# Performance work log

Hardware: AMD Instinct MI355X
Metric: run time of the kernel (lower is better)

## Reference

```python
import jax, jax.numpy as jnp
import numpy as np

# ---- config (CSA layer, layer_idx=0 of pattern 'CSA,HCA') ----
B, T, C = 2, 2048, 2048
NH, NKV = 16, 8
HD = C // NH            # 128 head dim
ROPE_DIM = HD // 2      # partial RoPE dims (rope_head_dim=0 default)
RATIO = 4               # csa_compress_ratio
G = T // RATIO          # compressed groups (T divisible by ratio -> no pad)
IDX_NH = NH
IDX_HD = max(8, C // NH // 2)  # 64
TOPK = 64               # index_topk
Q_RANK = C // 2         # _default_rank
O_RPG = C // 2          # o_proj rank_per_group, o_groups=1


def rms_norm(x, eps=1e-6):
    return x * jax.lax.rsqrt(jnp.mean(jnp.square(x), axis=-1, keepdims=True) + eps)


def _rope(x, cos, sin):
    d = x.shape[-1] // 2
    x1, x2 = x[..., :d], x[..., d:]
    return jnp.concatenate([x1 * cos + x2 * sin, -x1 * sin + x2 * cos], axis=-1)


def partial_rope(x, cos, sin):
    # rotate only the last ROPE_DIM dims; cos/sin: [..., ROPE_DIM//2]
    xn, xr = x[..., :-ROPE_DIM], x[..., -ROPE_DIM:]
    return jnp.concatenate([xn, _rope(xr, cos, sin)], axis=-1)


def setup_inputs() -> dict:
    key = jax.random.key(0)
    ks = jax.random.split(key, 16)
    s = 0.02
    x = jax.random.normal(ks[0], (B, T, C), jnp.float32)
    pos = jnp.arange(T, dtype=jnp.float32)
    inv = 10000.0 ** (-jnp.arange(0, HD // 2, dtype=jnp.float32) / (HD // 2))
    ang = pos[:, None] * inv[None, :]  # [T, HD//2]
    p = lambda i, shp: jax.random.normal(ks[i], shp, jnp.float32) * s
    return dict(
        x=x, cos=jnp.cos(ang), sin=jnp.sin(ang),
        q_a_w=p(1, (C, Q_RANK)), q_b_w=p(2, (Q_RANK, NH * HD)),
        ck_w=p(3, (C, NKV * HD)), cv_w=p(4, (C, NKV * HD)), cg_w=p(5, (C, NKV * HD)),
        c_ape=p(6, (RATIO, NKV, HD)),
        iq_w=p(7, (C, IDX_NH * IDX_HD)), ik_w=p(8, (C, IDX_NH * IDX_HD)),
        ig_w=p(9, (C, IDX_NH * IDX_HD)), i_ape=p(10, (RATIO, IDX_NH, IDX_HD)),
        sink=jnp.zeros((NH,), jnp.float32),
        o_wa=p(11, (1, O_RPG, C)), o_pb=p(12, (O_RPG, C)),
    )


def reference(x, cos, sin, q_a_w, q_b_w, ck_w, cv_w, cg_w, c_ape,
              iq_w, ik_w, ig_w, i_ape, sink, o_wa, o_pb):
    NEG = jnp.finfo(jnp.float32).min
    half = ROPE_DIM // 2
    # --- low-rank queries + partial RoPE ---
    q = (x @ q_a_w @ q_b_w).reshape(B, T, NH, HD)
    q = partial_rope(q, cos[None, :, None, :half], sin[None, :, None, :half])
    # --- GatedCompressor: learned gated pooling over blocks of RATIO ---
    k = (x @ ck_w).reshape(B, G, RATIO, NKV, HD)
    v = (x @ cv_w).reshape(B, G, RATIO, NKV, HD)
    g = (x @ cg_w).reshape(B, G, RATIO, NKV, HD) + c_ape[None, None]
    w = jax.nn.softmax(g, axis=2)
    ck = (k * w).sum(2)  # [B,G,NKV,HD]
    cv = (v * w).sum(2)
    group_ends = jnp.arange(RATIO - 1, T, RATIO)  # [G]
    ckr = partial_rope(ck, cos[group_ends][None, :, None, :half],
                       sin[group_ends][None, :, None, :half])
    # --- LightningIndexer: compressed indexer keys + per-token top-k groups ---
    ik = (x @ ik_w).reshape(B, G, RATIO, IDX_NH, IDX_HD)
    ig = (x @ ig_w).reshape(B, G, RATIO, IDX_NH, IDX_HD) + i_ape[None, None]
    iw = jax.nn.softmax(ig, axis=2)
    ikeys = rms_norm((ik * iw).sum(2))  # [B,G,IH,IHD]
    iq = rms_norm((x @ iq_w).reshape(B, T, IDX_NH, IDX_HD))
    iscore = jnp.einsum('bthd,bghd->bhtg', iq, ikeys) * IDX_HD ** -0.5
    iscore = iscore.mean(axis=1)  # [B,T,G]
    causal = group_ends[None, None, :] <= jnp.arange(T)[None, :, None]
    iscore = jnp.where(causal, iscore, NEG)
    sel = jax.lax.top_k(iscore, TOPK)[1]  # [B,T,K]
    bidx = jnp.arange(B)[:, None, None]
    tidx = jnp.arange(T)[None, :, None]
    mask = jnp.zeros((B, T, G), bool).at[bidx, tidx, sel].set(True) & causal
    # --- compressed sparse attention with sink, GQA expand ---
    rep = NH // NKV
    kk = jnp.repeat(ckr, rep, axis=2)  # [B,G,NH,HD]
    vv = jnp.repeat(cv, rep, axis=2)
    scores = jnp.einsum('bthd,bghd->bhtg', q, kk) * HD ** -0.5
    scores = jnp.where(mask[:, None], scores, NEG)
    sinkb = jnp.broadcast_to(sink.reshape(1, NH, 1, 1), (B, NH, T, 1))
    probs = jax.nn.softmax(jnp.concatenate([scores, sinkb], axis=-1), axis=-1)[..., :-1]
    out = jnp.einsum('bhtg,bghd->bthd', probs, vv).reshape(B, T, C)
    # --- GroupedOutputProjection (o_groups=1) ---
    h = jnp.einsum('btgd,grd->btgr', out.reshape(B, T, 1, C), o_wa).reshape(B, T, -1)
    return rms_norm(h) @ o_pb
```

## Files before the change

kernel.cpp:

```cpp
#include <hip/hip_runtime.h>
#include <hip/hip_bf16.h>
#include <math.h>

constexpr int Bn  = 2;
constexpr int Tn  = 2048;
constexpr int NHn = 16;
constexpr int NKVn= 8;
constexpr int Gn  = 512;
constexpr int TKn = 64;

typedef __attribute__((ext_vector_type(8))) __bf16 bf16x8;
typedef __attribute__((ext_vector_type(4))) __bf16 bf16x4;
typedef __attribute__((ext_vector_type(2))) __bf16 bf16x2;
typedef __attribute__((ext_vector_type(4))) float f32x4;

__device__ __forceinline__ void gload_lds16(const void* g, void* l) {
  __builtin_amdgcn_global_load_lds(
      (const __attribute__((address_space(1))) unsigned int*)g,
      (__attribute__((address_space(3))) unsigned int*)l, 16, 0, 0);
}

__global__ __launch_bounds__(256) void gemm_pipe_kvqa(
    const __bf16* __restrict__ A, const __bf16* __restrict__ Bt,
    float* __restrict__ Cf, __bf16* __restrict__ Cq)
{
  constexpr int K = 2048;
  constexpr int NT = K / 64;
  __shared__ __bf16 lds[2][2][2][128][32];
  const int tid = threadIdx.x;
  const int wid = tid >> 6, lane = tid & 63;
  const int wm = wid >> 1, wn = wid & 1;
  const int row0 = blockIdx.y * 128, col0 = blockIdx.x * 128;

  f32x4 acc[4][4];
  const f32x4 zero = {0.f, 0.f, 0.f, 0.f};
  #pragma unroll
  for (int i = 0; i < 4; ++i)
    #pragma unroll
    for (int j = 0; j < 4; ++j) acc[i][j] = zero;

  auto stage = [&](int kt, int p, int buf) {
    long k0 = (long)kt * 64 + p * 32;
    #pragma unroll
    for (int l = 0; l < 2; ++l) {
      int u = l * 256 + tid;
      int r = u >> 2, c4 = u & 3;
      long csrc = (long)((c4 ^ ((r >> 1) & 3)) * 8);
      gload_lds16(A  + (long)(row0 + r) * K + k0 + csrc, &lds[buf][0][p][r][c4 * 8]);
      gload_lds16(Bt + (long)(col0 + r) * K + k0 + csrc, &lds[buf][1][p][r][c4 * 8]);
    }
  };

  stage(0, 0, 0);
  stage(0, 1, 0);

  for (int kt = 0; kt < NT; ++kt) {
    const int buf = kt & 1;
    #pragma unroll
    for (int ph = 0; ph < 2; ++ph) {
      if (kt + 1 < NT) {
        stage(kt + 1, ph, buf ^ 1);
        asm volatile("s_waitcnt vmcnt(8)" ::: "memory");
      } else {
        if (ph == 0) asm volatile("s_waitcnt vmcnt(4)" ::: "memory");
        else         asm volatile("s_waitcnt vmcnt(0)" ::: "memory");
      }
      asm volatile("s_barrier" ::: "memory");
      bf16x8 af[4], bfr[4];
      #pragma unroll
      for (int mf = 0; mf < 4; ++mf) {
        int r = wm * 64 + mf * 16 + (lane & 15);
        int c4 = (lane >> 4) ^ ((r >> 1) & 3);
        af[mf] = *(const bf16x8*)&lds[buf][0][ph][r][c4 * 8];
      }
      #pragma unroll
      for (int nf = 0; nf < 4; ++nf) {
        int r = wn * 64 + nf * 16 + (lane & 15);
        int c4 = (lane >> 4) ^ ((r >> 1) & 3);
        bfr[nf] = *(const bf16x8*)&lds[buf][1][ph][r][c4 * 8];
      }
      __builtin_amdgcn_s_setprio(1);
      #pragma unroll
      for (int mf = 0; mf < 4; ++mf)
        #pragma unroll
        for (int nf = 0; nf < 4; ++nf)
          acc[mf][nf] = __builtin_amdgcn_mfma_f32_16x16x32_bf16(af[mf], bfr[nf], acc[mf][nf], 0, 0, 0);
      __builtin_amdgcn_s_setprio(0);
      asm volatile("s_barrier" ::: "memory");
    }
  }

  const int crow = (lane >> 4) * 4, ccol = lane & 15;
  const bool isQ = (col0 >= 3072);
  #pragma unroll
  for (int mf = 0; mf < 4; ++mf)
    #pragma unroll
    for (int nf = 0; nf < 4; ++nf)
      #pragma unroll
      for (int j = 0; j < 4; ++j) {
        long r = row0 + wm * 64 + mf * 16 + crow + j;
        long c = col0 + wn * 64 + nf * 16 + ccol;
        float v = acc[mf][nf][j];
        if (isQ) Cq[r * 1024 + (c - 3072)] = (__bf16)v;
        else     Cf[r * 3072 + c] = v;
      }
}

template<int EPI>
__global__ __launch_bounds__(256) void gemm_pipe(
    const __bf16* __restrict__ A, const __bf16* __restrict__ Bt,
    void* __restrict__ Cp, int N, int K,
    const float* __restrict__ cosb, const float* __restrict__ sinb,
    const float* __restrict__ rs)
{
  const int NT = K >> 6;
  __shared__ __bf16 lds[2][2][2][128][32];
  const int tid = threadIdx.x;
  const int wid = tid >> 6, lane = tid & 63;
  const int wm = wid >> 1, wn = wid & 1;
  const int row0 = blockIdx.y * 128, col0 = blockIdx.x * 128;

  f32x4 acc[4][4];
  const f32x4 zero = {0.f, 0.f, 0.f, 0.f};
  #pragma unroll
  for (int i = 0; i < 4; ++i)
    #pragma unroll
    for (int j = 0; j < 4; ++j) acc[i][j] = zero;

  auto stage = [&](int kt, int p, int buf) {
    long k0 = (long)kt * 64 + p * 32;
    #pragma unroll
    for (int l = 0; l < 2; ++l) {
      int u = l * 256 + tid;
      int r = u >> 2, c4 = u & 3;
      long csrc = (long)((c4 ^ ((r >> 1) & 3)) * 8);
      gload_lds16(A  + (long)(row0 + r) * K + k0 + csrc, &lds[buf][0][p][r][c4 * 8]);
      gload_lds16(Bt + (long)(col0 + r) * K + k0 + csrc, &lds[buf][1][p][r][c4 * 8]);
    }
  };

  stage(0, 0, 0);
  stage(0, 1, 0);

  for (int kt = 0; kt < NT; ++kt) {
    const int buf = kt & 1;
    #pragma unroll
    for (int ph = 0; ph < 2; ++ph) {
      if (kt + 1 < NT) {
        stage(kt + 1, ph, buf ^ 1);
        asm volatile("s_waitcnt vmcnt(8)" ::: "memory");
      } else {
        if (ph == 0) asm volatile("s_waitcnt vmcnt(4)" ::: "memory");
        else         asm volatile("s_waitcnt vmcnt(0)" ::: "memory");
      }
      asm volatile("s_barrier" ::: "memory");
      bf16x8 af[4], bfr[4];
      #pragma unroll
      for (int mf = 0; mf < 4; ++mf) {
        int r = wm * 64 + mf * 16 + (lane & 15);
        int c4 = (lane >> 4) ^ ((r >> 1) & 3);
        af[mf] = *(const bf16x8*)&lds[buf][0][ph][r][c4 * 8];
      }
      #pragma unroll
      for (int nf = 0; nf < 4; ++nf) {
        int r = wn * 64 + nf * 16 + (lane & 15);
        int c4 = (lane >> 4) ^ ((r >> 1) & 3);
        bfr[nf] = *(const bf16x8*)&lds[buf][1][ph][r][c4 * 8];
      }
      __builtin_amdgcn_s_setprio(1);
      #pragma unroll
      for (int mf = 0; mf < 4; ++mf)
        #pragma unroll
        for (int nf = 0; nf < 4; ++nf)
          acc[mf][nf] = __builtin_amdgcn_mfma_f32_16x16x32_bf16(af[mf], bfr[nf], acc[mf][nf], 0, 0, 0);
      __builtin_amdgcn_s_setprio(0);
      asm volatile("s_barrier" ::: "memory");
    }
  }

  const int crow = (lane >> 4) * 4, ccol = lane & 15;
  if constexpr (EPI == 1) {
    __bf16* C = (__bf16*)Cp;
    if (wn == 1) {
      #pragma unroll
      for (int mf = 0; mf < 4; ++mf)
        #pragma unroll
        for (int j = 0; j < 4; ++j) {
          long r = row0 + wm * 64 + mf * 16 + crow + j;
          int t = (int)(r & 2047);
          #pragma unroll
          for (int nfp = 0; nfp < 2; ++nfp) {
            int jj = nfp * 16 + ccol;
            float c = cosb[t * 64 + jj], s = sinb[t * 64 + jj];
            float x1 = acc[mf][nfp][j];
            float x2 = acc[mf][nfp + 2][j];
            C[r * N + col0 + 64 + jj] = (__bf16)(x1 * c + x2 * s);
            C[r * N + col0 + 96 + jj] = (__bf16)(-x1 * s + x2 * c);
          }
        }
    } else {
      #pragma unroll
      for (int mf = 0; mf < 4; ++mf)
        #pragma unroll
        for (int nf = 0; nf < 4; ++nf)
          #pragma unroll
          for (int j = 0; j < 4; ++j) {
            long r = row0 + wm * 64 + mf * 16 + crow + j;
            long c = col0 + nf * 16 + ccol;
            C[r * N + c] = (__bf16)acc[mf][nf][j];
          }
    }
  } else {
    #pragma unroll
    for (int mf = 0; mf < 4; ++mf)
      #pragma unroll
      for (int nf = 0; nf < 4; ++nf)
        #pragma unroll
        for (int j = 0; j < 4; ++j) {
          long r = row0 + wm * 64 + mf * 16 + crow + j;
          long c = col0 + wn * 64 + nf * 16 + ccol;
          float v = acc[mf][nf][j];
          if constexpr (EPI == 2)
            ((float*)Cp)[r * N + c] = v * rs[r];
          else
            ((__bf16*)Cp)[r * N + c] = (__bf16)v;
        }
  }
}

__global__ __launch_bounds__(256) void gemm_split(
    const __bf16* __restrict__ Ah, const __bf16* __restrict__ Al,
    const __bf16* __restrict__ Bh, const __bf16* __restrict__ Bl,
    float* __restrict__ C, int M, int N, int K, float alpha,
    long sA, long sB, long sC)
{
  const int NT = K >> 5;
  __shared__ __bf16 lds[2][4][128][32];
  const int tid = threadIdx.x;
  const int wid = tid >> 6, lane = tid & 63;
  const int wm = wid >> 1, wn = wid & 1;
  const int row0 = blockIdx.y * 128, col0 = blockIdx.x * 128;
  Ah += (long)blockIdx.z * sA;  Al += (long)blockIdx.z * sA;
  Bh += (long)blockIdx.z * sB;  Bl += (long)blockIdx.z * sB;

  f32x4 acc[4][4];
  const f32x4 zero = {0.f, 0.f, 0.f, 0.f};
  #pragma unroll
  for (int i = 0; i < 4; ++i)
    #pragma unroll
    for (int j = 0; j < 4; ++j) acc[i][j] = zero;

  auto stage = [&](int kt, int buf) {
    long k0 = (long)kt * 32;
    #pragma unroll
    for (int l = 0; l < 2; ++l) {
      int u = l * 256 + tid;
      int r = u >> 2, c4 = u & 3;
      long csrc = (long)((c4 ^ ((r >> 1) & 3)) * 8);
      long ga = (long)(row0 + r) * K + k0 + csrc;
      long gb = (long)(col0 + r) * K + k0 + csrc;
      gload_lds16(Ah + ga, &lds[buf][0][r][c4 * 8]);
      gload_lds16(Al + ga, &lds[buf][1][r][c4 * 8]);
      gload_lds16(Bh + gb, &lds[buf][2][r][c4 * 8]);
      gload_lds16(Bl + gb, &lds[buf][3][r][c4 * 8]);
    }
  };

  stage(0, 0);

  for (int kt = 0; kt < NT; ++kt) {
    const int buf = kt & 1;
    if (kt + 1 < NT) {
      stage(kt + 1, buf ^ 1);
      asm volatile("s_waitcnt vmcnt(8)" ::: "memory");
    } else {
      asm volatile("s_waitcnt vmcnt(0)" ::: "memory");
    }
    asm volatile("s_barrier" ::: "memory");
    bf16x8 ah[4], al[4], bh[4], bl[4];
    #pragma unroll
    for (int mf = 0; mf < 4; ++mf) {
      int r = wm * 64 + mf * 16 + (lane & 15);
      int c4 = (lane >> 4) ^ ((r >> 1) & 3);
      ah[mf] = *(const bf16x8*)&lds[buf][0][r][c4 * 8];
      al[mf] = *(const bf16x8*)&lds[buf][1][r][c4 * 8];
    }
    #pragma unroll
    for (int nf = 0; nf < 4; ++nf) {
      int r = wn * 64 + nf * 16 + (lane & 15);
      int c4 = (lane >> 4) ^ ((r >> 1) & 3);
      bh[nf] = *(const bf16x8*)&lds[buf][2][r][c4 * 8];
      bl[nf] = *(const bf16x8*)&lds[buf][3][r][c4 * 8];
    }
    __builtin_amdgcn_s_setprio(1);
    #pragma unroll
    for (int mf = 0; mf < 4; ++mf)
      #pragma unroll
      for (int nf = 0; nf < 4; ++nf) {
        acc[mf][nf] = __builtin_amdgcn_mfma_f32_16x16x32_bf16(ah[mf], bh[nf], acc[mf][nf], 0, 0, 0);
        acc[mf][nf] = __builtin_amdgcn_mfma_f32_16x16x32_bf16(ah[mf], bl[nf], acc[mf][nf], 0, 0, 0);
        acc[mf][nf] = __builtin_amdgcn_mfma_f32_16x16x32_bf16(al[mf], bh[nf], acc[mf][nf], 0, 0, 0);
      }
    __builtin_amdgcn_s_setprio(0);
    asm volatile("s_barrier" ::: "memory");
  }

  const int crow = (lane >> 4) * 4, ccol = lane & 15;
  #pragma unroll
  for (int mf = 0; mf < 4; ++mf)
    #pragma unroll
    for (int nf = 0; nf < 4; ++nf)
      #pragma unroll
      for (int j = 0; j < 4; ++j) {
        long r = row0 + wm * 64 + mf * 16 + crow + j;
        long c = col0 + wn * 64 + nf * 16 + ccol;
        C[(long)blockIdx.z * sC + r * N + c] = acc[mf][nf][j] * alpha;
      }
}

__global__ __launch_bounds__(256) void prep_index(
    const float* __restrict__ x,
    const float* __restrict__ s0, const float* __restrict__ s1,
    const float* __restrict__ s2,
    __bf16* __restrict__ hiB, __bf16* __restrict__ loB, long dstride,
    __bf16* __restrict__ xhi, __bf16* __restrict__ xlo)
{
  __shared__ float tile[64][65];
  int z = blockIdx.y;
  int tid = threadIdx.x;
  if (z < 3) {
    const int R = 2048, Cc = 1024;
    const float* in = (z == 0) ? s0 : (z == 1) ? s1 : s2;
    __bf16* hiT = hiB + (long)z * dstride;
    __bf16* loT = loB + (long)z * dstride;
    int f = blockIdx.x;
    int r0 = (f >> 4) * 64, c0 = (f & 15) * 64;
    #pragma unroll
    for (int j = 0; j < 16; ++j) {
      int idx = tid + j * 256;
      int r = idx >> 6, c = idx & 63;
      tile[r][c] = in[(long)(r0 + r) * Cc + c0 + c];
    }
    __syncthreads();
    #pragma unroll
    for (int j = 0; j < 16; ++j) {
      int idx = tid + j * 256;
      int c = idx >> 6, r = idx & 63;
      float v = tile[r][c];
      __bf16 h = (__bf16)v;
      hiT[(long)(c0 + c) * R + r0 + r] = h;
      loT[(long)(c0 + c) * R + r0 + r] = (__bf16)(v - (float)h);
    }
  } else {
    for (long i = ((long)blockIdx.x * 256 + tid) * 4; i < 8388608; i += 524288) {
      float4 v = *(const float4*)&x[i];
      bf16x4 h, l;
      h[0] = (__bf16)v.x; l[0] = (__bf16)(v.x - (float)h[0]);
      h[1] = (__bf16)v.y; l[1] = (__bf16)(v.y - (float)h[1]);
      h[2] = (__bf16)v.z; l[2] = (__bf16)(v.z - (float)h[2]);
      h[3] = (__bf16)v.w; l[3] = (__bf16)(v.w - (float)h[3]);
      *(bf16x4*)&xhi[i] = h;
      *(bf16x4*)&xlo[i] = l;
    }
  }
}

__global__ __launch_bounds__(256) void prep_main(
    const float* __restrict__ s0, const float* __restrict__ s1,
    const float* __restrict__ s2, const float* __restrict__ s3,
    const float* __restrict__ s4, const float* __restrict__ s5,
    const float* __restrict__ wa,
    __bf16* __restrict__ W, long W2, __bf16* __restrict__ owab)
{
  __shared__ float tile[64][65];
  int z = blockIdx.y;
  int tid = threadIdx.x;
  if (z < 6) {
    int R, Cc, r0, c0;
    const float* in;
    if (z < 4) {
      R = 2048; Cc = 1024;
      in = (z == 0) ? s0 : (z == 1) ? s1 : (z == 2) ? s2 : s3;
      r0 = (blockIdx.x >> 4) * 64; c0 = (blockIdx.x & 15) * 64;
    } else {
      R = 1024; Cc = 2048;
      in = (z == 4) ? s4 : s5;
      r0 = (blockIdx.x >> 5) * 64; c0 = (blockIdx.x & 31) * 64;
    }
    __bf16* out = W + (long)z * W2;
    #pragma unroll
    for (int j = 0; j < 16; ++j) {
      int idx = tid + j * 256;
      int r = idx >> 6, c = idx & 63;
      tile[r][c] = in[(long)(r0 + r) * Cc + c0 + c];
    }
    __syncthreads();
    #pragma unroll
    for (int j = 0; j < 16; ++j) {
      int idx = tid + j * 256;
      int c = idx >> 6, r = idx & 63;
      out[(long)(c0 + c) * R + r0 + r] = (__bf16)tile[r][c];
    }
  } else {
    for (long i = ((long)blockIdx.x * 256 + tid) * 4; i < 2097152; i += 524288) {
      float4 v = *(const float4*)&wa[i];
      bf16x4 o;
      o[0] = (__bf16)v.x; o[1] = (__bf16)v.y; o[2] = (__bf16)v.z; o[3] = (__bf16)v.w;
      *(bf16x4*)&owab[i] = o;
    }
  }
}

__global__ __launch_bounds__(256) void reduce_ckcv(
    const float* __restrict__ base, const float* __restrict__ c_ape,
    const float* __restrict__ cosb, const float* __restrict__ sinb,
    __bf16* __restrict__ ckb, __bf16* __restrict__ cvb)
{
  __shared__ float sck[256];
  const long S = 3072;
  int tid = threadIdx.x;
  int c = blockIdx.x * 256 + tid;
  int g = blockIdx.y, b = blockIdx.z;
  long row0 = (long)b * Tn + 4 * g;
  float lg[4], mx = -1e30f;
  #pragma unroll
  for (int r = 0; r < 4; ++r) {
    lg[r] = base[(row0 + r) * S + 2048 + c] + c_ape[r * 1024 + c];
    mx = fmaxf(mx, lg[r]);
  }
  float ssum = 0.f;
  #pragma unroll
  for (int r = 0; r < 4; ++r) { lg[r] = expf(lg[r] - mx); ssum += lg[r]; }
  float inv = 1.f / ssum, ak = 0.f, av = 0.f;
  #pragma unroll
  for (int r = 0; r < 4; ++r) {
    float w = lg[r] * inv;
    ak = fmaf(base[(row0 + r) * S + c],        w, ak);
    av = fmaf(base[(row0 + r) * S + 1024 + c], w, av);
  }
  long o = ((long)b * Gn + g) * 1024 + c;
  cvb[o] = (__bf16)av;
  sck[tid] = ak;
  __syncthreads();
  int d = c & 127;
  float outk = ak;
  if (d >= 64) {
    int t = 4 * g + 3;
    if (d < 96) {
      int j = d - 64;
      outk = ak * cosb[t * 64 + j] + sck[tid + 32] * sinb[t * 64 + j];
    } else {
      int j = d - 96;
      outk = -sck[tid - 32] * sinb[t * 64 + j] + ak * cosb[t * 64 + j];
    }
  }
  ckb[o] = (__bf16)outk;
}

__global__ __launch_bounds__(1024) void reduce_idx_fused(
    const float* __restrict__ base, const float* __restrict__ i_ape,
    __bf16* __restrict__ khi, __bf16* __restrict__ klo,
    __bf16* __restrict__ qhi, __bf16* __restrict__ qlo)
{
  const long S = 3072;
  int tid = threadIdx.x;
  int bid = blockIdx.x;
  if (bid < Gn * Bn) {
    int g = bid & (Gn - 1), b = bid >> 9;
    long row0 = (long)b * Tn + 4 * g;
    float lg[4], mx = -1e30f;
    #pragma unroll
    for (int r = 0; r < 4; ++r) {
      lg[r] = base[(row0 + r) * S + 1024 + tid] + i_ape[r * 1024 + tid];
      mx = fmaxf(mx, lg[r]);
    }
    float ssum = 0.f;
    #pragma unroll
    for (int r = 0; r < 4; ++r) { lg[r] = expf(lg[r] - mx); ssum += lg[r]; }
    float inv = 1.f / ssum, red = 0.f;
    #pragma unroll
    for (int r = 0; r < 4; ++r) red = fmaf(base[(row0 + r) * S + tid], lg[r] * inv, red);
    float ss = red * red;
    #pragma unroll
    for (int o = 32; o; o >>= 1) ss += __shfl_xor(ss, o);
    float v = red * rsqrtf(ss * (1.f / 64.f) + 1e-6f);
    long oi = ((long)b * Gn + g) * 1024 + tid;
    __bf16 h = (__bf16)v;
    khi[oi] = h; klo[oi] = (__bf16)(v - (float)h);
  } else {
    long row = bid - Gn * Bn;
    float v = base[row * S + 2048 + tid];
    float ss = v * v;
    #pragma unroll
    for (int o = 32; o; o >>= 1) ss += __shfl_xor(ss, o);
    float y = v * rsqrtf(ss * (1.f / 64.f) + 1e-6f);
    __bf16 h = (__bf16)y;
    qhi[row * 1024 + tid] = h;
    qlo[row * 1024 + tid] = (__bf16)(y - (float)h);
  }
}

__global__ __launch_bounds__(256) void rms_scales(
    const __bf16* __restrict__ h, float* __restrict__ rs)
{
  int wid = threadIdx.x >> 6, lane = threadIdx.x & 63;
  long row = (long)blockIdx.x * 4 + wid;
  const __bf16* hr = h + row * 1024 + lane * 16;
  bf16x8 a = *(const bf16x8*)hr;
  bf16x8 b = *(const bf16x8*)(hr + 8);
  float ss = 0.f;
  #pragma unroll
  for (int j = 0; j < 8; ++j) {
    float x = (float)a[j], y = (float)b[j];
    ss = fmaf(x, x, ss); ss = fmaf(y, y, ss);
  }
  #pragma unroll
  for (int o = 1; o < 64; o <<= 1) ss += __shfl_xor(ss, o);
  if (lane == 0) rs[row] = rsqrtf(ss * (1.f / 1024.f) + 1e-6f);
}

__global__ __launch_bounds__(256) void topk_kernel(
    const float* __restrict__ iscore, int* __restrict__ selidx, int* __restrict__ selcnt)
{
  int wave = threadIdx.x >> 6, lane = threadIdx.x & 63;
  long bt = (long)blockIdx.x * 4 + wave;
  int t = (int)(bt % Tn);
  const float* row = iscore + bt * Gn;
  int ng = (t + 1) >> 2; if (ng > Gn) ng = Gn;
  int cap = ng < TKn ? ng : TKn;
  float s[8];
  #pragma unroll
  for (int j = 0; j < 8; ++j) {
    int g = lane + 64 * j;
    s[j] = (g < ng) ? row[g] : -INFINITY;
  }
  int* outp = selidx + bt * TKn;
  for (int it = 0; it < cap; ++it) {
    float bv = -INFINITY; int bi = Gn;
    #pragma unroll
    for (int j = 0; j < 8; ++j) {
      int g = lane + 64 * j;
      if (s[j] > bv) { bv = s[j]; bi = g; }
    }
    #pragma unroll
    for (int o = 1; o < 64; o <<= 1) {
      float ov = __shfl_xor(bv, o); int oi = __shfl_xor(bi, o);
      if (ov > bv || (ov == bv && oi < bi)) { bv = ov; bi = oi; }
    }
    if (lane == 0) outp[it] = bi;
    #pragma unroll
    for (int j = 0; j < 8; ++j) if (bi == lane + 64 * j) s[j] = -INFINITY;
  }
  for (int it = cap + lane; it < TKn; it += 64) outp[it] = 0;
  if (lane == 0) selcnt[bt] = cap;
}

__global__ __launch_bounds__(256) void attn_kernel(
    const __bf16* __restrict__ q, const __bf16* __restrict__ ckb,
    const __bf16* __restrict__ cvb, const int* __restrict__ selidx,
    const int* __restrict__ selcnt, const float* __restrict__ sink,
    __bf16* __restrict__ out)
{
  __shared__ float sS[4][16][68];
  __shared__ int   sG[4][64];
  const float scale = 0.08838834764831845f;
  int wid = threadIdx.x >> 6, lane = threadIdx.x & 63;
  long bt = (long)blockIdx.x * 4 + wid;
  int b = (int)(bt >> 11);
  int cnt = selcnt[bt];
  int gid = (lane < cnt) ? selidx[bt * TKn + lane] : 0;
  sG[wid][lane] = gid;

  int grp = lane >> 3;
  int sub = lane & 7;
  int h0 = grp * 2, h1 = h0 + 1;
  int d0 = sub * 16;

  const __bf16* qrow = q + bt * 2048;
  float q0[16], q1[16];
  {
    bf16x8 a0 = *(const bf16x8*)&qrow[h0 * 128 + d0];
    bf16x8 a1 = *(const bf16x8*)&qrow[h0 * 128 + d0 + 8];
    bf16x8 c0 = *(const bf16x8*)&qrow[h1 * 128 + d0];
    bf16x8 c1 = *(const bf16x8*)&qrow[h1 * 128 + d0 + 8];
    #pragma unroll
    for (int j = 0; j < 8; ++j) {
      q0[j] = (float)a0[j]; q0[8 + j] = (float)a1[j];
      q1[j] = (float)c0[j]; q1[8 + j] = (float)c1[j];
    }
  }
  __syncthreads();

  for (int i0 = 0; i0 < 64; i0 += 8) {
    #pragma unroll
    for (int u = 0; u < 8; ++u) {
      int i = i0 + u;
      int g = sG[wid][i];
      const __bf16* kr = ckb + ((long)(b * Gn + g)) * 1024 + lane * 16;
      bf16x8 k0 = *(const bf16x8*)kr;
      bf16x8 k1 = *(const bf16x8*)(kr + 8);
      float p0 = 0.f, p1 = 0.f;
      #pragma unroll
      for (int j = 0; j < 8; ++j) {
        float kv = (float)k0[j];
        p0 = fmaf(kv, q0[j], p0); p1 = fmaf(kv, q1[j], p1);
      }
      #pragma unroll
      for (int j = 0; j < 8; ++j) {
        float kv = (float)k1[j];
        p0 = fmaf(kv, q0[8 + j], p0); p1 = fmaf(kv, q1[8 + j], p1);
      }
      p0 += __shfl_xor(p0, 1); p0 += __shfl_xor(p0, 2); p0 += __shfl_xor(p0, 4);
      p1 += __shfl_xor(p1, 1); p1 += __shfl_xor(p1, 2); p1 += __shfl_xor(p1, 4);
      if (sub == 0) { sS[wid][h0][i] = p0; sS[wid][h1][i] = p1; }
    }
  }
  __syncthreads();

  {
    int h = lane >> 2, qtr = lane & 3;
    float sv[16];
    float mx = -INFINITY;
    #pragma unroll
    for (int j = 0; j < 16; ++j) {
      int i = qtr * 16 + j;
      float s = (i < cnt) ? sS[wid][h][i] * scale : -INFINITY;
      sv[j] = s; mx = fmaxf(mx, s);
    }
    mx = fmaxf(mx, __shfl_xor(mx, 1));
    mx = fmaxf(mx, __shfl_xor(mx, 2));
    float snk = sink[h];
    mx = fmaxf(mx, snk);
    float sum = 0.f;
    #pragma unroll
    for (int j = 0; j < 16; ++j) { sv[j] = __expf(sv[j] - mx); sum += sv[j]; }
    sum += __shfl_xor(sum, 1);
    sum += __shfl_xor(sum, 2);
    sum += __expf(snk - mx);
    float inv = 1.f / sum;
    #pragma unroll
    for (int j = 0; j < 16; ++j) sS[wid][h][qtr * 16 + j] = sv[j] * inv;
  }
  __syncthreads();

  float o0[16], o1[16];
  #pragma unroll
  for (int j = 0; j < 16; ++j) { o0[j] = 0.f; o1[j] = 0.f; }
  for (int i0 = 0; i0 < 64; i0 += 8) {
    #pragma unroll
    for (int u = 0; u < 8; ++u) {
      int i = i0 + u;
      int g = sG[wid][i];
      float p0 = sS[wid][h0][i], p1 = sS[wid][h1][i];
      const __bf16* vr = cvb + ((long)(b * Gn + g)) * 1024 + lane * 16;
      bf16x8 v0 = *(const bf16x8*)vr;
      bf16x8 v1 = *(const bf16x8*)(vr + 8);
      #pragma unroll
      for (int j = 0; j < 8; ++j) {
        float vv = (float)v0[j];
        o0[j] = fmaf(p0, vv, o0[j]); o1[j] = fmaf(p1, vv, o1[j]);
      }
      #pragma unroll
      for (int j = 0; j < 8; ++j) {
        float vv = (float)v1[j];
        o0[8 + j] = fmaf(p0, vv, o0[8 + j]); o1[8 + j] = fmaf(p1, vv, o1[8 + j]);
      }
    }
  }
  __bf16* ob = out + bt * 2048;
  bf16x8 w;
  #pragma unroll
  for (int j = 0; j < 8; ++j) w[j] = (__bf16)o0[j];
  *(bf16x8*)&ob[h0 * 128 + d0] = w;
  #pragma unroll
  for (int j = 0; j < 8; ++j) w[j] = (__bf16)o0[8 + j];
  *(bf16x8*)&ob[h0 * 128 + d0 + 8] = w;
  #pragma unroll
  for (int j = 0; j < 8; ++j) w[j] = (__bf16)o1[j];
  *(bf16x8*)&ob[h1 * 128 + d0] = w;
  #pragma unroll
  for (int j = 0; j < 8; ++j) w[j] = (__bf16)o1[8 + j];
  *(bf16x8*)&ob[h1 * 128 + d0 + 8] = w;
}

extern "C" void kernel_launch(void* const* d_in, const int* in_sizes, int n_in,
                              void* d_out, int out_size, void* d_ws, size_t ws_size,
                              hipStream_t stream) {
  const float* x     = (const float*)d_in[0];
  const float* cosb  = (const float*)d_in[1];
  const float* sinb  = (const float*)d_in[2];
  const float* q_a_w = (const float*)d_in[3];
  const float* q_b_w = (const float*)d_in[4];
  const float* ck_w  = (const float*)d_in[5];
  const float* cv_w  = (const float*)d_in[6];
  const float* cg_w  = (const float*)d_in[7];
  const float* c_ape = (const float*)d_in[8];
  const float* iq_w  = (const float*)d_in[9];
  const float* ik_w  = (const float*)d_in[10];
  const float* ig_w  = (const float*)d_in[11];
  const float* i_ape = (const float*)d_in[12];
  const float* sink  = (const float*)d_in[13];
  const float* o_wa  = (const float*)d_in[14];
  const float* o_pb  = (const float*)d_in[15];
  float* outp = (float*)d_out;
  float* ws = (float*)d_ws;

  const long F  = 4194304;
  const long M1 = 1048576;

  float* b_all = ws;
  float*  iscore = ws + F;
  __bf16* oatt_b = (__bf16*)(ws + F);
  __bf16* hb_b   = (__bf16*)ws;

  __bf16* iq_hi = (__bf16*)d_out;
  __bf16* iq_lo = (__bf16*)d_out + 4194304;
  __bf16* qb    = (__bf16*)d_out;

  char* tp = (char*)(ws + 3 * F);
  __bf16* ckb = (__bf16*)tp;     tp += (size_t)M1 * 4;
  __bf16* cvb = (__bf16*)tp;     tp += (size_t)M1 * 4;
  int*   selidx = (int*)tp;      tp += 2097152;
  int*   selcnt = selidx + Bn * Tn * TKn;
  __bf16* ikeys_hi = (__bf16*)tp; tp += 2097152;
  __bf16* ikeys_lo = (__bf16*)tp; tp += 2097152;
  __bf16* xhi = (__bf16*)tp;      tp += 16777216;
  __bf16* xlo = (__bf16*)tp;      tp += 16777216;
  __bf16* W   = (__bf16*)tp;      tp += 7 * 4194304;
  __bf16* qa_buf = (__bf16*)tp;   tp += 8388608;
  float*  rs     = (float*)tp;    tp += 16384;
  const long W2 = 2097152;
  __bf16* Whi = W;            __bf16* Wlo = W + 3 * W2;
  __bf16* ckT  = W;
  __bf16* qbT  = W + 4*W2;
  __bf16* opbT = W + 5*W2;   __bf16* owab = W + 6*W2;

  prep_index<<<dim3(512, 4), 256, 0, stream>>>(
      x, ik_w, ig_w, iq_w, Whi, Wlo, W2, xhi, xlo);

  gemm_split<<<dim3(24, 32), 256, 0, stream>>>(xhi, xlo, Whi, Wlo, b_all,
      4096, 3072, 2048, 1.f, 0, 0, 0);
  reduce_idx_fused<<<dim3(Gn * Bn + Bn * Tn), 1024, 0, stream>>>(
      b_all, i_ape, ikeys_hi, ikeys_lo, iq_hi, iq_lo);

  gemm_split<<<dim3(4, 16, 2), 256, 0, stream>>>(iq_hi, iq_lo, ikeys_hi, ikeys_lo, iscore,
      2048, 512, 1024, 1.f / 128.f, (long)2048 * 1024, (long)512 * 1024, (long)2048 * 512);
  topk_kernel<<<dim3(Bn * Tn / 4), 256, 0, stream>>>(iscore, selidx, selcnt);

  prep_main<<<dim3(512, 7), 256, 0, stream>>>(
      ck_w, cv_w, cg_w, q_a_w, q_b_w, o_pb, o_wa, W, W2, owab);

  gemm_pipe_kvqa<<<dim3(32, 32), 256, 0, stream>>>(xhi, ckT, b_all, qa_buf);
  reduce_ckcv<<<dim3(4, Gn, Bn), 256, 0, stream>>>(b_all, c_ape, cosb, sinb, ckb, cvb);

  gemm_pipe<1><<<dim3(16, 32), 256, 0, stream>>>(
      qa_buf, qbT, qb, 2048, 1024, cosb, sinb, nullptr);

  attn_kernel<<<dim3(Bn * Tn / 4), 256, 0, stream>>>(qb, ckb, cvb, selidx, selcnt, sink, oatt_b);

  gemm_pipe<0><<<dim3(8, 32), 256, 0, stream>>>(
      oatt_b, owab, hb_b, 1024, 2048, nullptr, nullptr, nullptr);
  rms_scales<<<dim3(1024), 256, 0, stream>>>(hb_b, rs);
  gemm_pipe<2><<<dim3(16, 32), 256, 0, stream>>>(
      hb_b, opbT, outp, 2048, 1024, nullptr, nullptr, rs);
}
```

Measured before the change: 541.8 us.

## Enlarge kvqa GEMM to 256x256 tiles with 8-wave, 8-phase interleaved pipeline

The fused K/V/gate/q_a projection GEMM now uses 256x256 output tiles with 512 threads (8 waves, each covering a 128x64 sub-tile). Each K step is split into four sub-phases that interleave the LDS fragment reads, the async global-to-LDS prefetch of the next tile, and the MFMA blocks, with explicit waitcnt, barrier and sched_barrier placement. The aim is more data reuse per byte loaded and better overlap of memory with matrix math. The cost is double the LDS (64KB), more accumulator registers, and a grid of only 256 blocks, which may under-fill the GPU's compute units.

```diff
diff --git a/kernel.cpp b/kernel.cpp
--- a/kernel.cpp
+++ b/kernel.cpp
@@ -20,85 +20,156 @@
       (__attribute__((address_space(3))) unsigned int*)l, 16, 0, 0);
 }
 
-__global__ __launch_bounds__(256) void gemm_pipe_kvqa(
+__global__ __launch_bounds__(512) void gemm_kvqa_8ph(
     const __bf16* __restrict__ A, const __bf16* __restrict__ Bt,
     float* __restrict__ Cf, __bf16* __restrict__ Cq)
 {
   constexpr int K = 2048;
   constexpr int NT = K / 64;
-  __shared__ __bf16 lds[2][2][2][128][32];
+  __shared__ __bf16 lds[2][2][2][256][32];
   const int tid = threadIdx.x;
   const int wid = tid >> 6, lane = tid & 63;
-  const int wm = wid >> 1, wn = wid & 1;
-  const int row0 = blockIdx.y * 128, col0 = blockIdx.x * 128;
-
-  f32x4 acc[4][4];
+  const int wm = wid >> 2, wn = wid & 3;
+  const int row0 = blockIdx.y * 256, col0 = blockIdx.x * 256;
+
+  f32x4 acc[8][4];
   const f32x4 zero = {0.f, 0.f, 0.f, 0.f};
   #pragma unroll
-  for (int i = 0; i < 4; ++i)
+  for (int i = 0; i < 8; ++i)
     #pragma unroll
     for (int j = 0; j < 4; ++j) acc[i][j] = zero;
 
-  auto stage = [&](int kt, int p, int buf) {
-    long k0 = (long)kt * 64 + p * 32;
+  auto stage1 = [&](int kt, int op, int ph, int buf) {
+    long k0 = (long)kt * 64 + ph * 32;
+    const __bf16* src = op ? Bt : A;
+    const int base0 = op ? col0 : row0;
     #pragma unroll
     for (int l = 0; l < 2; ++l) {
-      int u = l * 256 + tid;
+      int u = l * 512 + tid;
       int r = u >> 2, c4 = u & 3;
       long csrc = (long)((c4 ^ ((r >> 1) & 3)) * 8);
-      gload_lds16(A  + (long)(row0 + r) * K + k0 + csrc, &lds[buf][0][p][r][c4 * 8]);
-      gload_lds16(Bt + (long)(col0 + r) * K + k0 + csrc, &lds[buf][1][p][r][c4 * 8]);
+      gload_lds16(src + (long)(base0 + r) * K + k0 + csrc, &lds[buf][op][ph][r][c4 * 8]);
     }
   };
 
-  stage(0, 0, 0);
-  stage(0, 1, 0);
+  stage1(0, 0, 0, 0);
+  stage1(0, 1, 0, 0);
+  stage1(0, 0, 1, 0);
+  stage1(0, 1, 1, 0);
+  asm volatile("s_waitcnt vmcnt(4)" ::: "memory");
+  asm volatile("s_barrier" ::: "memory");
 
   for (int kt = 0; kt < NT; ++kt) {
     const int buf = kt & 1;
-    #pragma unroll
-    for (int ph = 0; ph < 2; ++ph) {
-      if (kt + 1 < NT) {
-        stage(kt + 1, ph, buf ^ 1);
-        asm volatile("s_waitcnt vmcnt(8)" ::: "memory");
-      } else {
-        if (ph == 0) asm volatile("s_waitcnt vmcnt(4)" ::: "memory");
-        else         asm volatile("s_waitcnt vmcnt(0)" ::: "memory");
-      }
-      asm volatile("s_barrier" ::: "memory");
-      bf16x8 af[4], bfr[4];
-      #pragma unroll
-      for (int mf = 0; mf < 4; ++mf) {
-        int r = wm * 64 + mf * 16 + (lane & 15);
-        int c4 = (lane >> 4) ^ ((r >> 1) & 3);
-        af[mf] = *(const bf16x8*)&lds[buf][0][ph][r][c4 * 8];
-      }
-      #pragma unroll
-      for (int nf = 0; nf < 4; ++nf) {
-        int r = wn * 64 + nf * 16 + (lane & 15);
-        int c4 = (lane >> 4) ^ ((r >> 1) & 3);
-        bfr[nf] = *(const bf16x8*)&lds[buf][1][ph][r][c4 * 8];
-      }
-      __builtin_amdgcn_s_setprio(1);
-      #pragma unroll
-      for (int mf = 0; mf < 4; ++mf)
-        #pragma unroll
-        for (int nf = 0; nf < 4; ++nf)
-          acc[mf][nf] = __builtin_amdgcn_mfma_f32_16x16x32_bf16(af[mf], bfr[nf], acc[mf][nf], 0, 0, 0);
-      __builtin_amdgcn_s_setprio(0);
-      asm volatile("s_barrier" ::: "memory");
-    }
+    const bool pre = (kt + 1 < NT);
+    bf16x8 afA[4], afB[4], bf[4];
+
+    #pragma unroll
+    for (int i = 0; i < 4; ++i) {
+      int r = wm * 128 + i * 16 + (lane & 15);
+      int c4 = (lane >> 4) ^ ((r >> 1) & 3);
+      afA[i] = *(const bf16x8*)&lds[buf][0][0][r][c4 * 8];
+    }
+    #pragma unroll
+    for (int i = 0; i < 4; ++i) {
+      int r = wn * 64 + i * 16 + (lane & 15);
+      int c4 = (lane >> 4) ^ ((r >> 1) & 3);
+      bf[i] = *(const bf16x8*)&lds[buf][1][0][r][c4 * 8];
+    }
+    if (pre) stage1(kt + 1, 0, 0, buf ^ 1);
+    asm volatile("s_barrier" ::: "memory");
+    asm volatile("s_waitcnt lgkmcnt(0)" ::: "memory");
+    __builtin_amdgcn_sched_barrier(0);
+    __builtin_amdgcn_s_setprio(1);
+    #pragma unroll
+    for (int i = 0; i < 4; ++i)
+      #pragma unroll
+      for (int j = 0; j < 4; ++j)
+        acc[i][j] = __builtin_amdgcn_mfma_f32_16x16x32_bf16(afA[i], bf[j], acc[i][j], 0, 0, 0);
+    __builtin_amdgcn_s_setprio(0);
+    asm volatile("s_barrier" ::: "memory");
+
+    #pragma unroll
+    for (int i = 0; i < 4; ++i) {
+      int r = wm * 128 + (i + 4) * 16 + (lane & 15);
+      int c4 = (lane >> 4) ^ ((r >> 1) & 3);
+      afB[i] = *(const bf16x8*)&lds[buf][0][0][r][c4 * 8];
+    }
+    if (pre) {
+      stage1(kt + 1, 1, 0, buf ^ 1);
+      asm volatile("s_waitcnt vmcnt(4)" ::: "memory");
+    } else {
+      asm volatile("s_waitcnt vmcnt(0)" ::: "memory");
+    }
+    asm volatile("s_barrier" ::: "memory");
+    asm volatile("s_waitcnt lgkmcnt(0)" ::: "memory");
+    __builtin_amdgcn_sched_barrier(0);
+    __builtin_amdgcn_s_setprio(1);
+    #pragma unroll
+    for (int i = 0; i < 4; ++i)
+      #pragma unroll
+      for (int j = 0; j < 4; ++j)
+        acc[i + 4][j] = __builtin_amdgcn_mfma_f32_16x16x32_bf16(afB[i], bf[j], acc[i + 4][j], 0, 0, 0);
+    __builtin_amdgcn_s_setprio(0);
+    asm volatile("s_barrier" ::: "memory");
+
+    #pragma unroll
+    for (int i = 0; i < 4; ++i) {
+      int r = wm * 128 + i * 16 + (lane & 15);
+      int c4 = (lane >> 4) ^ ((r >> 1) & 3);
+      afA[i] = *(const bf16x8*)&lds[buf][0][1][r][c4 * 8];
+    }
+    #pragma unroll
+    for (int i = 0; i < 4; ++i) {
+      int r = wn * 64 + i * 16 + (lane & 15);
+      int c4 = (lane >> 4) ^ ((r >> 1) & 3);
+      bf[i] = *(const bf16x8*)&lds[buf][1][1][r][c4 * 8];
+    }
+    if (pre) stage1(kt + 1, 0, 1, buf ^ 1);
+    asm volatile("s_barrier" ::: "memory");
+    asm volatile("s_waitcnt lgkmcnt(0)" ::: "memory");
+    __builtin_amdgcn_sched_barrier(0);
+    __builtin_amdgcn_s_setprio(1);
+    #pragma unroll
+    for (int i = 0; i < 4; ++i)
+      #pragma unroll
+      for (int j = 0; j < 4; ++j)
+        acc[i][j] = __builtin_amdgcn_mfma_f32_16x16x32_bf16(afA[i], bf[j], acc[i][j], 0, 0, 0);
+    __builtin_amdgcn_s_setprio(0);
+    asm volatile("s_barrier" ::: "memory");
+
+    #pragma unroll
+    for (int i = 0; i < 4; ++i) {
+      int r = wm * 128 + (i + 4) * 16 + (lane & 15);
+      int c4 = (lane >> 4) ^ ((r >> 1) & 3);
+      afB[i] = *(const bf16x8*)&lds[buf][0][1][r][c4 * 8];
+    }
+    if (pre) {
+      stage1(kt + 1, 1, 1, buf ^ 1);
+      asm volatile("s_waitcnt vmcnt(4)" ::: "memory");
+    }
+    asm volatile("s_barrier" ::: "memory");
+    asm volatile("s_waitcnt lgkmcnt(0)" ::: "memory");
+    __builtin_amdgcn_sched_barrier(0);
+    __builtin_amdgcn_s_setprio(1);
+    #pragma unroll
+    for (int i = 0; i < 4; ++i)
+      #pragma unroll
+      for (int j = 0; j < 4; ++j)
+        acc[i + 4][j] = __builtin_amdgcn_mfma_f32_16x16x32_bf16(afB[i], bf[j], acc[i + 4][j], 0, 0, 0);
+    __builtin_amdgcn_s_setprio(0);
+    asm volatile("s_barrier" ::: "memory");
   }
 
   const int crow = (lane >> 4) * 4, ccol = lane & 15;
   const bool isQ = (col0 >= 3072);
   #pragma unroll
-  for (int mf = 0; mf < 4; ++mf)
+  for (int mf = 0; mf < 8; ++mf)
     #pragma unroll
     for (int nf = 0; nf < 4; ++nf)
       #pragma unroll
       for (int j = 0; j < 4; ++j) {
-        long r = row0 + wm * 64 + mf * 16 + crow + j;
+        long r = row0 + wm * 128 + mf * 16 + crow + j;
         long c = col0 + wn * 64 + nf * 16 + ccol;
         float v = acc[mf][nf][j];
         if (isQ) Cq[r * 1024 + (c - 3072)] = (__bf16)v;
@@ -750,7 +821,7 @@
   prep_main<<<dim3(512, 7), 256, 0, stream>>>(
       ck_w, cv_w, cg_w, q_a_w, q_b_w, o_pb, o_wa, W, W2, owab);
 
-  gemm_pipe_kvqa<<<dim3(32, 32), 256, 0, stream>>>(xhi, ckT, b_all, qa_buf);
+  gemm_kvqa_8ph<<<dim3(16, 16), 512, 0, stream>>>(xhi, ckT, b_all, qa_buf);
   reduce_ckcv<<<dim3(4, Gn, Bn), 256, 0, stream>>>(b_all, c_ape, cosb, sinb, ckb, cvb);
 
   gemm_pipe<1><<<dim3(16, 32), 256, 0, stream>>>(
```

New measurement: 525.1 us. 1.03x faster.
